# Kernel tuning notes

Hardware: AMD Instinct MI355X
Metric: run time of the kernel (lower is better)

Reference implementation:

```python
import jax, jax.numpy as jnp
import numpy as np
from jax import lax

B, N, S, H = 8, 32, 512, 768   # batch, max spans, seq len, bert hidden
K, C, L = 3, 128, 64           # conv kernel height, cnn_hidden_size, num labels


def setup_inputs() -> dict:
    key = jax.random.key(0)
    ks = jax.random.split(key, 9)
    rng = np.random.default_rng(0)
    W = 16  # max span width
    starts = rng.integers(0, S - W, size=(B, N))
    widths = rng.integers(1, W + 1, size=(B, N))
    starts[0, 0], widths[0, 0] = 100, W        # force max span width = 16
    starts[0, 1], widths[0, 1] = S - W, 1      # force max prefix width = 496
    starts[0, 2], widths[0, 2] = 0, 1          # force min end = 1 -> max suffix = 511
    ends = starts + widths
    spans_dranges = jnp.asarray(np.stack([starts, ends], axis=-1), dtype=jnp.int32)
    sc = 0.02
    return {
        "tokens_emb": jax.random.normal(ks[0], (B, S, H), jnp.float32),
        "span_w": jax.random.normal(ks[1], (C, H, K), jnp.float32) * sc,
        "span_b": jax.random.normal(ks[2], (C,), jnp.float32) * sc,
        "prefix_w": jax.random.normal(ks[3], (C, H, K), jnp.float32) * sc,
        "prefix_b": jax.random.normal(ks[4], (C,), jnp.float32) * sc,
        "suffix_w": jax.random.normal(ks[5], (C, H, K), jnp.float32) * sc,
        "suffix_b": jax.random.normal(ks[6], (C,), jnp.float32) * sc,
        "fc_w": jax.random.normal(ks[7], (L, 3 * C), jnp.float32) * sc,
        "fc_b": jax.random.normal(ks[8], (L,), jnp.float32) * sc,
        "spans_dranges": spans_dranges,
        "word_seq_lengths": jnp.full((B,), S, dtype=jnp.int32),
        "max_span_width": W,
        "max_prefix_width": S - W,
        "max_suffix_width": S - 1,
    }


def _conv_pool(x, w, b):
    # x: [BN, T, H]; Conv2d(H->C, kernel (K,1)) over time + max_pool over all valid positions
    T = x.shape[1]
    if T < K:  # original pads with zeros up to kernel size
        x = jnp.pad(x, ((0, 0), (0, K - T), (0, 0)))
    y = lax.conv_general_dilated(x.transpose(0, 2, 1), w, (1,), 'VALID',
                                 dimension_numbers=('NCH', 'OIH', 'NCH'))  # [BN, C, T-K+1]
    return (y + b[None, :, None]).max(axis=2)  # pool_filter_size == full output length


def reference(tokens_emb, span_w, span_b, prefix_w, prefix_b, suffix_w, suffix_b,
              fc_w, fc_b, spans_dranges, word_seq_lengths,
              max_span_width, max_prefix_width, max_suffix_width):
    starts = spans_dranges[..., 0]  # [B,N]
    ends = spans_dranges[..., 1]

    def gather(idx, mask):
        # idx, mask: [B,N,W] -> zero-padded per-span token embeddings [B*N, W, H]
        g = jnp.take_along_axis(tokens_emb[:, None], jnp.clip(idx, 0, S - 1)[..., None], axis=2)
        return (g * mask[..., None]).reshape(B * N, -1, H)

    ar = jnp.arange(max_span_width)
    span_x = gather(starts[..., None] + ar, ar < (ends - starts)[..., None])
    arp = jnp.arange(max_prefix_width)
    prefix_x = gather(jnp.broadcast_to(arp, (B, N, max_prefix_width)), arp < starts[..., None])
    ars = jnp.arange(max_suffix_width)
    suffix_x = gather(ends[..., None] + ars,
                      ars < (word_seq_lengths[:, None, None] - ends[..., None]))

    feats = jnp.concatenate([
        _conv_pool(prefix_x, prefix_w, prefix_b),
        _conv_pool(span_x, span_w, span_b),
        _conv_pool(suffix_x, suffix_w, suffix_b),
    ], axis=-1)  # [B*N, 3C]
    probs = jax.nn.sigmoid(feats @ fc_w.T + fc_b)  # [B*N, L]
    pred_ids = (probs > 0.5).astype(jnp.int32).reshape(B, N, L)
    return probs, pred_ids
```

## Files before the change

kernel.cpp:

```cpp
#include <hip/hip_runtime.h>
#include <hip/hip_bf16.h>
#include <math.h>

#define NEG_INF (-1e30f)

typedef _Float16 half8 __attribute__((ext_vector_type(8)));
typedef _Float16 half4 __attribute__((ext_vector_type(4)));
typedef float f32x4 __attribute__((ext_vector_type(4)));
typedef float f32x16 __attribute__((ext_vector_type(16)));

__global__ __launch_bounds__(256) void prep(
    const float* __restrict__ tokens, const float* __restrict__ span_w,
    const float* __restrict__ prefix_w, const float* __restrict__ suffix_w,
    const float* __restrict__ fc_w, _Float16* __restrict__ A2f,
    _Float16* __restrict__ Btf, float* __restrict__ fcT) {
  int bid = blockIdx.x;
  int t = threadIdx.x;
  if (bid < 3072) {
    int g4 = (bid * 256 + t) * 4;
    int m = g4 / 768, h = g4 % 768;
    float4 x = *(const float4*)(tokens + g4);
    float xs[4] = {x.x, x.y, x.z, x.w};
    half4 hi, lo;
#pragma unroll
    for (int i = 0; i < 4; ++i) {
      _Float16 h_ = (_Float16)xs[i];
      hi[i] = h_;
      lo[i] = (_Float16)((xs[i] - (float)h_) * 64.0f);
    }
    const int mt = m >> 5;
    const int lane = (m & 31) + 32 * ((h >> 3) & 1);
    const int j0 = h & 7;
    const size_t base = ((size_t)mt * 96 + (h >> 4)) * 512 + lane * 8 + j0;
    *(half4*)(A2f + base) = hi;
    *(half4*)(A2f + base + (size_t)48 * 512) = lo;
  } else if (bid < 3216) {
    int g = (bid - 3072) * 256 + t;
    int ws = g / 12288;
    int r = g % 12288;
    int c = r / 96, h = (r % 96) * 8;
    const float* wsrc = (ws == 0) ? prefix_w : (ws == 1) ? span_w : suffix_w;
    const float* src = wsrc + (size_t)(c * 768 + h) * 3;
    float wv[24];
#pragma unroll
    for (int i = 0; i < 6; ++i) *(float4*)&wv[i * 4] = *(const float4*)(src + i * 4);
#pragma unroll
    for (int tap = 0; tap < 3; ++tap) {
      half8 hi, lo;
#pragma unroll
      for (int i = 0; i < 8; ++i) {
        float x = wv[i * 3 + tap];
        _Float16 h_ = (_Float16)x;
        hi[i] = h_;
        lo[i] = (_Float16)((x - (float)h_) * 64.0f);
      }
      const int n = ws * 384 + tap * 128 + c;
      const int nt = n >> 5;
      const int lane = (n & 31) + 32 * ((h >> 3) & 1);
      const size_t base = ((size_t)nt * 96 + (h >> 4)) * 512 + lane * 8;
      *(half8*)(Btf + base) = hi;
      *(half8*)(Btf + base + (size_t)48 * 512) = lo;
    }
  } else {
    int g = (bid - 3216) * 256 + t;
    int i = g >> 6, c = g & 63;
    fcT[g] = fc_w[c * 384 + i];
  }
}

__global__ __launch_bounds__(256) void gemm_f16(const _Float16* __restrict__ A2f,
                                                const _Float16* __restrict__ Btf,
                                                float* __restrict__ Ct) {
  const int w = threadIdx.x >> 6;
  const int lane = threadIdx.x & 63;
  const int mt = blockIdx.x * 4 + w;
  const int nt0 = blockIdx.y * 2;
  const _Float16* pa = A2f + (size_t)mt * 49152 + lane * 8;
  const _Float16* pb0 = Btf + (size_t)nt0 * 49152 + lane * 8;
  const _Float16* pb1 = pb0 + 49152;
  f32x16 aa0, ab0, aa1, ab1;
#pragma unroll
  for (int q = 0; q < 16; ++q) {
    aa0[q] = 0.f;
    ab0[q] = 0.f;
    aa1[q] = 0.f;
    ab1[q] = 0.f;
  }
#pragma unroll 2
  for (int kt = 0; kt < 48; ++kt) {
    const int o0 = kt * 512;
    const int o1 = o0 + 48 * 512;
    half8 a0 = *(const half8*)(pa + o0);
    half8 a1 = *(const half8*)(pa + o1);
    half8 b00 = *(const half8*)(pb0 + o0);
    half8 b01 = *(const half8*)(pb0 + o1);
    half8 b10 = *(const half8*)(pb1 + o0);
    half8 b11 = *(const half8*)(pb1 + o1);
    aa0 = __builtin_amdgcn_mfma_f32_32x32x16_f16(a0, b00, aa0, 0, 0, 0);
    aa1 = __builtin_amdgcn_mfma_f32_32x32x16_f16(a0, b10, aa1, 0, 0, 0);
    ab0 = __builtin_amdgcn_mfma_f32_32x32x16_f16(a1, b00, ab0, 0, 0, 0);
    ab1 = __builtin_amdgcn_mfma_f32_32x32x16_f16(a1, b10, ab1, 0, 0, 0);
    ab0 = __builtin_amdgcn_mfma_f32_32x32x16_f16(a0, b01, ab0, 0, 0, 0);
    ab1 = __builtin_amdgcn_mfma_f32_32x32x16_f16(a0, b11, ab1, 0, 0, 0);
  }
  const int l31 = lane & 31;
  const int hi32 = lane >> 5;
  const int m0 = mt * 32 + 4 * hi32;
  {
    const int n_out = nt0 * 32 + l31;
    float* cp = Ct + (size_t)n_out * 4096 + m0;
#pragma unroll
    for (int r = 0; r < 4; ++r) {
      f32x4 v;
#pragma unroll
      for (int q = 0; q < 4; ++q) v[q] = aa0[4 * r + q] + 0.015625f * ab0[4 * r + q];
      *(f32x4*)(cp + 8 * r) = v;
    }
  }
  {
    const int n_out = (nt0 + 1) * 32 + l31;
    float* cp = Ct + (size_t)n_out * 4096 + m0;
#pragma unroll
    for (int r = 0; r < 4; ++r) {
      f32x4 v;
#pragma unroll
      for (int q = 0; q < 4; ++q) v[q] = aa1[4 * r + q] + 0.015625f * ab1[4 * r + q];
      *(f32x4*)(cp + 8 * r) = v;
    }
  }
}

__global__ __launch_bounds__(256) void scan_kernel(const float* __restrict__ Ct,
                                                   const int* __restrict__ wsl,
                                                   float* __restrict__ PM2,
                                                   float* __restrict__ SM2) {
  int pair = blockIdx.x * 4 + (threadIdx.x >> 6);
  int b = pair >> 7;
  int c = pair & 127;
  int lane = threadIdx.x & 63;
  int mb = b * 512;
  int t0 = lane * 8;
  const float* p0 = Ct + (size_t)(0 + c) * 4096 + mb;
  const float* p1 = Ct + (size_t)(128 + c) * 4096 + mb;
  const float* p2 = Ct + (size_t)(256 + c) * 4096 + mb;
  float v[8];
#pragma unroll
  for (int i = 0; i < 8; i++) {
    int t = t0 + i;
    v[i] = (t < 494) ? (p0[t] + p1[t + 1] + p2[t + 2]) : NEG_INF;
  }
#pragma unroll
  for (int i = 1; i < 8; i++) v[i] = fmaxf(v[i], v[i - 1]);
  float x = v[7];
#pragma unroll
  for (int d = 1; d < 64; d <<= 1) {
    float y = __shfl_up(x, d);
    if (lane >= d) x = fmaxf(x, y);
  }
  float excl = __shfl_up(x, 1);
  if (lane == 0) excl = NEG_INF;
  float* pm = PM2 + (size_t)pair * 512;
#pragma unroll
  for (int i = 0; i < 8; i++) {
    int t = t0 + i;
    if (t < 494) pm[t] = fmaxf(v[i], excl);
  }
  const float* s0 = Ct + (size_t)(768 + c) * 4096 + mb;
  const float* s1 = Ct + (size_t)(896 + c) * 4096 + mb;
  const float* s2 = Ct + (size_t)(1024 + c) * 4096 + mb;
  int qmax = wsl[b] - 3;
  if (qmax > 509) qmax = 509;
  float u[8];
#pragma unroll
  for (int i = 0; i < 8; i++) {
    int q = t0 + i;
    u[i] = (q <= qmax) ? (s0[q] + s1[q + 1] + s2[q + 2]) : NEG_INF;
  }
#pragma unroll
  for (int i = 6; i >= 0; i--) u[i] = fmaxf(u[i], u[i + 1]);
  float xr = u[0];
#pragma unroll
  for (int d = 1; d < 64; d <<= 1) {
    float y = __shfl_down(xr, d);
    if (lane < 64 - d) xr = fmaxf(xr, y);
  }
  float exclr = __shfl_down(xr, 1);
  if (lane == 63) exclr = NEG_INF;
  float* sm = SM2 + (size_t)pair * 512;
#pragma unroll
  for (int i = 0; i < 8; i++) sm[t0 + i] = fmaxf(u[i], exclr);
}

__global__ __launch_bounds__(128) void span_kernel(
    const float* __restrict__ Ct, const float* __restrict__ PM2,
    const float* __restrict__ SM2, const float* __restrict__ prefix_b,
    const float* __restrict__ span_b, const float* __restrict__ suffix_b,
    const float* __restrict__ fcT, const float* __restrict__ fc_b,
    const int* __restrict__ spans, const int* __restrict__ wsl,
    float* __restrict__ out) {
  __shared__ float sfeat[384];
  __shared__ float part[64];
  int sp = blockIdx.x;
  int b = sp >> 5;
  int c = threadIdx.x;
  int s = spans[sp * 2], e = spans[sp * 2 + 1];
  int Lb = wsl[b];
  int mb = b * 512;
  {
    const float* t0p = Ct + (size_t)c * 4096 + mb;
    const float* t1p = Ct + (size_t)(128 + c) * 4096 + mb;
    float m = NEG_INF;
    if (s >= 3) m = fmaxf(m, PM2[(size_t)(b * 128 + c) * 512 + s - 3]);
    if (s >= 2 && s <= 495) m = fmaxf(m, t0p[s - 2] + t1p[s - 1]);
    if (s >= 1 && s <= 494) m = fmaxf(m, t0p[s - 1]);
    if (s <= 493) m = fmaxf(m, 0.0f);
    sfeat[c] = m + prefix_b[c];
  }
  {
    const float* u0 = Ct + (size_t)(384 + c) * 4096 + mb;
    const float* u1 = Ct + (size_t)(512 + c) * 4096 + mb;
    const float* u2 = Ct + (size_t)(640 + c) * 4096 + mb;
    int w = e - s;
    float m = NEG_INF;
    for (int p = 0; p + 2 < w; ++p)
      m = fmaxf(m, u0[s + p] + u1[s + p + 1] + u2[s + p + 2]);
    if (w >= 2 && w <= 15) m = fmaxf(m, u0[s + w - 2] + u1[s + w - 1]);
    if (w <= 14) m = fmaxf(m, u0[s + w - 1]);
    if (w <= 13) m = fmaxf(m, 0.0f);
    sfeat[128 + c] = m + span_b[c];
  }
  {
    const float* x0 = Ct + (size_t)(768 + c) * 4096 + mb;
    const float* x1 = Ct + (size_t)(896 + c) * 4096 + mb;
    float m = NEG_INF;
    if (e <= Lb - 3) m = fmaxf(m, SM2[(size_t)(b * 128 + c) * 512 + e]);
    if (Lb - 2 - e >= 0 && Lb - 2 - e <= 508)
      m = fmaxf(m, x0[Lb - 2] + x1[Lb - 1]);
    if (Lb - 1 - e >= 0 && Lb - 1 - e <= 508) m = fmaxf(m, x0[Lb - 1]);
    if (Lb - e <= 508) m = fmaxf(m, 0.0f);
    sfeat[256 + c] = m + suffix_b[c];
  }
  __syncthreads();
  {
    int cc = threadIdx.x & 63;
    int half = threadIdx.x >> 6;
    float acc2 = 0.0f;
    const float* fp = fcT + (size_t)(half * 192) * 64 + cc;
    const float* sf = sfeat + half * 192;
#pragma unroll 8
    for (int i = 0; i < 192; ++i) acc2 = fmaf(sf[i], fp[(size_t)i * 64], acc2);
    if (half) part[cc] = acc2;
    __syncthreads();
    if (!half) {
      float a = acc2 + part[cc] + fc_b[cc];
      float pr = 1.0f / (1.0f + expf(-a));
      out[sp * 64 + cc] = pr;
      out[16384 + sp * 64 + cc] = (pr > 0.5f) ? 1.0f : 0.0f;
    }
  }
}

extern "C" void kernel_launch(void* const* d_in, const int* in_sizes, int n_in,
                              void* d_out, int out_size, void* d_ws,
                              size_t ws_size, hipStream_t stream) {
  const float* tokens = (const float*)d_in[0];
  const float* span_w = (const float*)d_in[1];
  const float* span_b = (const float*)d_in[2];
  const float* prefix_w = (const float*)d_in[3];
  const float* prefix_b = (const float*)d_in[4];
  const float* suffix_w = (const float*)d_in[5];
  const float* suffix_b = (const float*)d_in[6];
  const float* fc_w = (const float*)d_in[7];
  const float* fc_b = (const float*)d_in[8];
  const int* spans = (const int*)d_in[9];
  const int* wsl = (const int*)d_in[10];
  float* out = (float*)d_out;

  char* ws = (char*)d_ws;
  float* Ct = (float*)ws;
  _Float16* A2f = (_Float16*)(ws + 18874368);
  _Float16* Btf = (_Float16*)(ws + 31457280);
  float* PM2 = (float*)(ws + 34996224);
  float* SM2 = (float*)(ws + 37093376);
  float* fcT = (float*)(ws + 39190528);

  hipLaunchKernelGGL(prep, dim3(3312), dim3(256), 0, stream, tokens, span_w,
                     prefix_w, suffix_w, fc_w, A2f, Btf, fcT);
  hipLaunchKernelGGL(gemm_f16, dim3(32, 18), dim3(256), 0, stream, A2f, Btf, Ct);
  hipLaunchKernelGGL(scan_kernel, dim3(256), dim3(256), 0, stream, Ct, wsl,
                     PM2, SM2);
  hipLaunchKernelGGL(span_kernel, dim3(256), dim3(128), 0, stream, Ct, PM2,
                     SM2, prefix_b, span_b, suffix_b, fcT, fc_b, spans, wsl,
                     out);
}
```

Measured before the change: 165.3 us.

## Split GEMM K dimension four ways and sum partials in consumers

The GEMM grid gains a z dimension of 4, and each block handles a quarter of the K loop and writes its own partial output slab in the workspace. The scan and span kernels now sum the four partial slabs on every read of Ct. The aim is more parallelism: the original grid launched only 576 blocks for the long K loop on a GPU with many CUs. The cost is four times the Ct write traffic and four times the reads in the consumer kernels, plus a larger workspace.

```diff
diff --git a/kernel.cpp b/kernel.cpp
--- a/kernel.cpp
+++ b/kernel.cpp
@@ -3,6 +3,10 @@
 #include <math.h>
 
 #define NEG_INF (-1e30f)
+#define CT_PART 4718592
+#define CS(P, i)                                              \
+  (((P)[i] + (P)[CT_PART + (i)]) +                            \
+   ((P)[2 * CT_PART + (i)] + (P)[3 * CT_PART + (i)]))
 
 typedef _Float16 half8 __attribute__((ext_vector_type(8)));
 typedef _Float16 half4 __attribute__((ext_vector_type(4)));
@@ -75,8 +79,9 @@
   const int lane = threadIdx.x & 63;
   const int mt = blockIdx.x * 4 + w;
   const int nt0 = blockIdx.y * 2;
-  const _Float16* pa = A2f + (size_t)mt * 49152 + lane * 8;
-  const _Float16* pb0 = Btf + (size_t)nt0 * 49152 + lane * 8;
+  const int kz = blockIdx.z;
+  const _Float16* pa = A2f + (size_t)mt * 49152 + (size_t)kz * 12 * 512 + lane * 8;
+  const _Float16* pb0 = Btf + (size_t)nt0 * 49152 + (size_t)kz * 12 * 512 + lane * 8;
   const _Float16* pb1 = pb0 + 49152;
   f32x16 aa0, ab0, aa1, ab1;
 #pragma unroll
@@ -86,8 +91,8 @@
     aa1[q] = 0.f;
     ab1[q] = 0.f;
   }
-#pragma unroll 2
-  for (int kt = 0; kt < 48; ++kt) {
+#pragma unroll 3
+  for (int kt = 0; kt < 12; ++kt) {
     const int o0 = kt * 512;
     const int o1 = o0 + 48 * 512;
     half8 a0 = *(const half8*)(pa + o0);
@@ -106,9 +111,10 @@
   const int l31 = lane & 31;
   const int hi32 = lane >> 5;
   const int m0 = mt * 32 + 4 * hi32;
+  float* outC = Ct + (size_t)kz * CT_PART;
   {
     const int n_out = nt0 * 32 + l31;
-    float* cp = Ct + (size_t)n_out * 4096 + m0;
+    float* cp = outC + (size_t)n_out * 4096 + m0;
 #pragma unroll
     for (int r = 0; r < 4; ++r) {
       f32x4 v;
@@ -119,7 +125,7 @@
   }
   {
     const int n_out = (nt0 + 1) * 32 + l31;
-    float* cp = Ct + (size_t)n_out * 4096 + m0;
+    float* cp = outC + (size_t)n_out * 4096 + m0;
 #pragma unroll
     for (int r = 0; r < 4; ++r) {
       f32x4 v;
@@ -147,7 +153,7 @@
 #pragma unroll
   for (int i = 0; i < 8; i++) {
     int t = t0 + i;
-    v[i] = (t < 494) ? (p0[t] + p1[t + 1] + p2[t + 2]) : NEG_INF;
+    v[i] = (t < 494) ? (CS(p0, t) + CS(p1, t + 1) + CS(p2, t + 2)) : NEG_INF;
   }
 #pragma unroll
   for (int i = 1; i < 8; i++) v[i] = fmaxf(v[i], v[i - 1]);
@@ -174,7 +180,7 @@
 #pragma unroll
   for (int i = 0; i < 8; i++) {
     int q = t0 + i;
-    u[i] = (q <= qmax) ? (s0[q] + s1[q + 1] + s2[q + 2]) : NEG_INF;
+    u[i] = (q <= qmax) ? (CS(s0, q) + CS(s1, q + 1) + CS(s2, q + 2)) : NEG_INF;
   }
 #pragma unroll
   for (int i = 6; i >= 0; i--) u[i] = fmaxf(u[i], u[i + 1]);
@@ -211,8 +217,8 @@
     const float* t1p = Ct + (size_t)(128 + c) * 4096 + mb;
     float m = NEG_INF;
     if (s >= 3) m = fmaxf(m, PM2[(size_t)(b * 128 + c) * 512 + s - 3]);
-    if (s >= 2 && s <= 495) m = fmaxf(m, t0p[s - 2] + t1p[s - 1]);
-    if (s >= 1 && s <= 494) m = fmaxf(m, t0p[s - 1]);
+    if (s >= 2 && s <= 495) m = fmaxf(m, CS(t0p, s - 2) + CS(t1p, s - 1));
+    if (s >= 1 && s <= 494) m = fmaxf(m, CS(t0p, s - 1));
     if (s <= 493) m = fmaxf(m, 0.0f);
     sfeat[c] = m + prefix_b[c];
   }
@@ -223,9 +229,9 @@
     int w = e - s;
     float m = NEG_INF;
     for (int p = 0; p + 2 < w; ++p)
-      m = fmaxf(m, u0[s + p] + u1[s + p + 1] + u2[s + p + 2]);
-    if (w >= 2 && w <= 15) m = fmaxf(m, u0[s + w - 2] + u1[s + w - 1]);
-    if (w <= 14) m = fmaxf(m, u0[s + w - 1]);
+      m = fmaxf(m, CS(u0, s + p) + CS(u1, s + p + 1) + CS(u2, s + p + 2));
+    if (w >= 2 && w <= 15) m = fmaxf(m, CS(u0, s + w - 2) + CS(u1, s + w - 1));
+    if (w <= 14) m = fmaxf(m, CS(u0, s + w - 1));
     if (w <= 13) m = fmaxf(m, 0.0f);
     sfeat[128 + c] = m + span_b[c];
   }
@@ -235,8 +241,8 @@
     float m = NEG_INF;
     if (e <= Lb - 3) m = fmaxf(m, SM2[(size_t)(b * 128 + c) * 512 + e]);
     if (Lb - 2 - e >= 0 && Lb - 2 - e <= 508)
-      m = fmaxf(m, x0[Lb - 2] + x1[Lb - 1]);
-    if (Lb - 1 - e >= 0 && Lb - 1 - e <= 508) m = fmaxf(m, x0[Lb - 1]);
+      m = fmaxf(m, CS(x0, Lb - 2) + CS(x1, Lb - 1));
+    if (Lb - 1 - e >= 0 && Lb - 1 - e <= 508) m = fmaxf(m, CS(x0, Lb - 1));
     if (Lb - e <= 508) m = fmaxf(m, 0.0f);
     sfeat[256 + c] = m + suffix_b[c];
   }
@@ -278,15 +284,16 @@
 
   char* ws = (char*)d_ws;
   float* Ct = (float*)ws;
-  _Float16* A2f = (_Float16*)(ws + 18874368);
-  _Float16* Btf = (_Float16*)(ws + 31457280);
-  float* PM2 = (float*)(ws + 34996224);
-  float* SM2 = (float*)(ws + 37093376);
-  float* fcT = (float*)(ws + 39190528);
+  _Float16* A2f = (_Float16*)(ws + 75497472);
+  _Float16* Btf = (_Float16*)(ws + 88080384);
+  float* PM2 = (float*)(ws + 91619328);
+  float* SM2 = (float*)(ws + 93716480);
+  float* fcT = (float*)(ws + 95813632);
 
   hipLaunchKernelGGL(prep, dim3(3312), dim3(256), 0, stream, tokens, span_w,
                      prefix_w, suffix_w, fc_w, A2f, Btf, fcT);
-  hipLaunchKernelGGL(gemm_f16, dim3(32, 18), dim3(256), 0, stream, A2f, Btf, Ct);
+  hipLaunchKernelGGL(gemm_f16, dim3(32, 18, 4), dim3(256), 0, stream, A2f, Btf,
+                     Ct);
   hipLaunchKernelGGL(scan_kernel, dim3(256), dim3(256), 0, stream, Ct, wsl,
                      PM2, SM2);
   hipLaunchKernelGGL(span_kernel, dim3(256), dim3(128), 0, stream, Ct, PM2,
```

New measurement: 205.7 us. 1.24x slower.
